# Performance work log

Hardware: AMD Instinct MI355X
Metric: run time of the kernel (lower is better)

## Reference

```python
import jax, jax.numpy as jnp
import numpy as np

DMODEL = 1024
NUM_HEADS = 16
HEAD_DIM = DMODEL // NUM_HEADS


def setup_inputs() -> dict:
    key = jax.random.key(0)
    k_x, k_wqkv, k_bqkv, k_wo, k_bo = jax.random.split(key, 5)
    B, T, D = 4, 2048, DMODEL
    s = 1.0 / np.sqrt(D)
    return {
        "x": jax.random.normal(k_x, (B, T, D), dtype=jnp.float32),
        "w_qkv": jax.random.uniform(k_wqkv, (D, 3 * D), dtype=jnp.float32, minval=-s, maxval=s),
        "b_qkv": jax.random.uniform(k_bqkv, (3 * D,), dtype=jnp.float32, minval=-s, maxval=s),
        "w_out": jax.random.uniform(k_wo, (D, D), dtype=jnp.float32, minval=-s, maxval=s),
        "b_out": jax.random.uniform(k_bo, (D,), dtype=jnp.float32, minval=-s, maxval=s),
    }


def reference(x, w_qkv, b_qkv, w_out, b_out):
    B, T, D = x.shape
    H, Hd = NUM_HEADS, HEAD_DIM
    qkv = x @ w_qkv + b_qkv                      # [B,T,3D]
    qkv = qkv.reshape(B, T, 3, H, Hd)
    q = jnp.transpose(qkv[:, :, 0], (0, 2, 1, 3))  # [B,H,T,Hd]
    k = jnp.transpose(qkv[:, :, 1], (0, 2, 1, 3))
    v = jnp.transpose(qkv[:, :, 2], (0, 2, 1, 3))
    scores = jnp.einsum("bhqd,bhkd->bhqk", q, k) / jnp.sqrt(jnp.float32(Hd))
    weights = jax.nn.softmax(scores, axis=-1)
    attn = jnp.einsum("bhqk,bhkd->bhqd", weights, v)  # [B,H,T,Hd]
    attn = jnp.transpose(attn, (0, 2, 1, 3)).reshape(B, T, D)
    return attn @ w_out + b_out
```

## Files before the change

### kernel.cpp

```cpp
#include <hip/hip_runtime.h>
#include <hip/hip_bf16.h>


typedef __bf16 bf16_t;
typedef __bf16 bf16x8 __attribute__((ext_vector_type(8)));
typedef float f32x4 __attribute__((ext_vector_type(4)));
typedef short short4v __attribute__((ext_vector_type(4)));

#if __has_builtin(__builtin_amdgcn_mfma_f32_16x16x16_bf16)
typedef __bf16 bf16x4 __attribute__((ext_vector_type(4)));
#define MFMA_PV(va, vb, c) __builtin_amdgcn_mfma_f32_16x16x16_bf16( \
    __builtin_bit_cast(bf16x4, (va)), __builtin_bit_cast(bf16x4, (vb)), (c), 0, 0, 0)
#else
#define MFMA_PV(va, vb, c) __builtin_amdgcn_mfma_f32_16x16x16bf16_1k((va), (vb), (c), 0, 0, 0)
#endif

#define DMODEL 1024
#define NH     16
#define HD     64
#define BATCH  4
#define SEQ    2048
#define NTOK   (BATCH * SEQ)
#define NOUT   (NTOK * DMODEL)
#define CEXP   0.1803368801111204f

__device__ __forceinline__ void async_ld16(void* lds, const void* g) {
  __builtin_amdgcn_global_load_lds(
      (const __attribute__((address_space(1))) void*)g,
      (__attribute__((address_space(3))) void*)lds, 16, 0, 0);
}

__global__ __launch_bounds__(256) void sniff_dtype(
    const uint4* __restrict__ x, int* __restrict__ flag,
    const void* __restrict__ sq, const void* __restrict__ so,
    float* __restrict__ dq, float* __restrict__ dofs) {
  int t = threadIdx.x;
  int nanish = 0, zc = 0;
  for (int j = 0; j < 4; ++j) {
    uint4 w = x[t + j * 256];
    unsigned u[4] = {w.x, w.y, w.z, w.w};
    for (int k = 0; k < 4; ++k) {
      unsigned lo = u[k] & 0xFFFFu, hi = u[k] >> 16;
      if ((lo & 0x7F80u) == 0x7F80u) nanish++;
      if ((hi & 0x7F80u) == 0x7F80u) nanish++;
      if (lo == 0) zc++;
      if (hi == 0) zc++;
    }
  }
  __shared__ int rn[256], rz[256];
  rn[t] = nanish; rz[t] = zc;
  __syncthreads();
  for (int s = 128; s > 0; s >>= 1) {
    if (t < s) { rn[t] += rn[t + s]; rz[t] += rz[t + s]; }
    __syncthreads();
  }
  const int f = (rn[0] > 4 || rz[0] > 2048) ? 1 : 0;
  if (t == 0) flag[0] = f;
  for (int j = 0; j < 16; ++j) {
    int i = j * 256 + t;
    if (i < 3072)
      dq[i] = f ? ((const float*)sq)[i] : (float)((const bf16_t*)sq)[i];
    else {
      int k = i - 3072;
      dofs[k] = f ? ((const float*)so)[k] : (float)((const bf16_t*)so)[k];
    }
  }
}

__global__ __launch_bounds__(256) void conv_to_bf16(
    const void* __restrict__ src, bf16_t* __restrict__ dst, int n,
    const int* __restrict__ flag) {
  int i = (blockIdx.x * 256 + threadIdx.x) * 8;
  if (i >= n) return;
  if (flag[0]) {
    const float4* s = (const float4*)((const float*)src + i);
    float4 a = s[0], b = s[1];
    bf16_t* o = dst + i;
    o[0] = (bf16_t)a.x; o[1] = (bf16_t)a.y; o[2] = (bf16_t)a.z; o[3] = (bf16_t)a.w;
    o[4] = (bf16_t)b.x; o[5] = (bf16_t)b.y; o[6] = (bf16_t)b.z; o[7] = (bf16_t)b.w;
  } else {
    *(uint4*)(dst + i) = *(const uint4*)((const bf16_t*)src + i);
  }
}

__global__ __launch_bounds__(256) void transpose_w2(
    const void* __restrict__ in0, bf16_t* __restrict__ out0,
    const void* __restrict__ in1, bf16_t* __restrict__ out1,
    const int* __restrict__ flag) {
  __shared__ bf16_t tile[32][33];
  const int tx = threadIdx.x & 31, ty = threadIdx.x >> 5;
  const bool second = blockIdx.x >= 96;
  const void* in = second ? in1 : in0;
  bf16_t* out = second ? out1 : out0;
  const int C = second ? 1024 : 3072;
  const int R = 1024;
  const int c0 = (second ? (blockIdx.x - 96) : blockIdx.x) * 32;
  const int r0 = blockIdx.y * 32;
  if (flag[0]) {
    for (int i = 0; i < 4; ++i) {
      int r = ty + i * 8;
      tile[r][tx] = (bf16_t)((const float*)in)[(size_t)(r0 + r) * C + c0 + tx];
    }
  } else {
    for (int i = 0; i < 4; ++i) {
      int r = ty + i * 8;
      tile[r][tx] = ((const bf16_t*)in)[(size_t)(r0 + r) * C + c0 + tx];
    }
  }
  __syncthreads();
  for (int i = 0; i < 4; ++i) {
    int r = ty + i * 8;
    out[(size_t)(c0 + r) * R + r0 + tx] = tile[tx][r];
  }
}

template <int MODE>
__global__ __launch_bounds__(256) void gemm_bt_bias(
    const bf16_t* __restrict__ A, const bf16_t* __restrict__ Bt,
    const float* __restrict__ bias, void* __restrict__ Cout,
    int M, int N, int K, const int* __restrict__ flag) {
  __shared__ bf16_t sA[2][128 * 32];
  __shared__ bf16_t sB[2][128 * 32];
  const int t = threadIdx.x;
  const int wave = t >> 6, lane = t & 63;
  const int quad = lane >> 4, l16 = lane & 15;
  const int nwg = gridDim.x * gridDim.y;
  const int lin = blockIdx.y * gridDim.x + blockIdx.x;
  const int cpx = nwg >> 3;
  const int swz = (lin & 7) * cpx + (lin >> 3);
  const int bx = swz % gridDim.x, by = swz / gridDim.x;
  const int bM = by * 128, bN = bx * 128;
  const int m0w = (wave >> 1) * 64, n0w = (wave & 1) * 64;
  const int rowS = wave * 16 + (lane >> 2);
  const int kcS = (lane & 3) * 8;

  f32x4 acc[4][4] = {};

  auto stage = [&](int buf, int k0) {
    for (int r = 0; r < 2; ++r) {
      int row = r * 64 + rowS;
      async_ld16((char*)sA[buf] + r * 4096 + wave * 1024,
                 A + (size_t)(bM + row) * K + k0 + kcS);
      async_ld16((char*)sB[buf] + r * 4096 + wave * 1024,
                 Bt + (size_t)(bN + row) * K + k0 + kcS);
    }
  };

  const int nsteps = K >> 5;
  stage(0, 0);

  for (int s = 0; s < nsteps; ++s) {
    const int cur = s & 1;
    if (s + 1 < nsteps) {
      stage(cur ^ 1, (s + 1) << 5);
      asm volatile("s_waitcnt vmcnt(4)" ::: "memory");
    } else {
      asm volatile("s_waitcnt vmcnt(0)" ::: "memory");
    }
    __builtin_amdgcn_s_barrier();
    asm volatile("" ::: "memory");

    bf16x8 af[4], bfr[4];
    for (int i = 0; i < 4; ++i)
      af[i] = *(const bf16x8*)&sA[cur][(m0w + i * 16 + l16) * 32 + quad * 8];
    for (int j = 0; j < 4; ++j)
      bfr[j] = *(const bf16x8*)&sB[cur][(n0w + j * 16 + l16) * 32 + quad * 8];
    for (int i = 0; i < 4; ++i)
      for (int j = 0; j < 4; ++j)
        acc[i][j] = __builtin_amdgcn_mfma_f32_16x16x32_bf16(af[i], bfr[j], acc[i][j], 0, 0, 0);

    asm volatile("" ::: "memory");
    __builtin_amdgcn_s_barrier();
  }

  const bool f32out = (MODE == 1) && flag[0];
  for (int j = 0; j < 4; ++j) {
    int col = bN + n0w + j * 16 + l16;
    float bv = bias[col];
    for (int i = 0; i < 4; ++i) {
      int row0 = bM + m0w + i * 16 + quad * 4;
      for (int r = 0; r < 4; ++r) {
        float v = acc[i][j][r] + bv;
        if (f32out) ((float*)Cout)[(size_t)(row0 + r) * N + col] = v;
        else        ((bf16_t*)Cout)[(size_t)(row0 + r) * N + col] = (bf16_t)v;
      }
    }
  }
}

__global__ __launch_bounds__(512) void gemm256_qkv(
    const bf16_t* __restrict__ A, const bf16_t* __restrict__ Bt,
    const float* __restrict__ bias, bf16_t* __restrict__ Cout,
    int M, int N, int K, bf16_t* __restrict__ vT) {
  __shared__ __align__(16) char smem[131072];
  char* lds = smem;
  const int t = threadIdx.x;
  const int wave = t >> 6, lane = t & 63;
  const int quad = lane >> 4, l16 = lane & 15;
  const int wr = wave >> 2, wc = wave & 3;
  const int nwg = gridDim.x * gridDim.y;
  const int lin = blockIdx.y * gridDim.x + blockIdx.x;
  const int cpx = nwg >> 3;
  const int swzb = (lin & 7) * cpx + (lin >> 3);
  const int bx = swzb % gridDim.x, by = swzb / gridDim.x;
  const int bM = by * 256, bN = bx * 256;

  const int srow = t >> 2;
  const int xr = ((srow >> 3) & 1) | (((srow >> 2) & 1) << 1);
  const int skl = ((t ^ xr) & 3) * 8;
  const size_t offA0 = (size_t)(bM + srow) * K + skl;
  const size_t offB0 = (size_t)(bN + srow) * K + skl;
  const size_t off1 = (size_t)128 * K;
  const int ldsw = wave * 1024;

#define STG_A(bufo, h, k0t) do {                                               \
    async_ld16(lds + (bufo) + (h) * 16384 + ldsw, A + offA0 + (k0t) + (h) * 32);\
    async_ld16(lds + (bufo) + (h) * 16384 + 8192 + ldsw,                       \
               A + offA0 + off1 + (k0t) + (h) * 32); } while (0)
#define STG_B(bufo, h, k0t) do {                                               \
    async_ld16(lds + (bufo) + 32768 + (h) * 16384 + ldsw,                      \
               Bt + offB0 + (k0t) + (h) * 32);                                 \
    async_ld16(lds + (bufo) + 32768 + (h) * 16384 + 8192 + ldsw,               \
               Bt + offB0 + off1 + (k0t) + (h) * 32); } while (0)

  int aoff[8], boff[4];
#pragma unroll
  for (int mf = 0; mf < 8; ++mf) {
    int r = wr * 128 + mf * 16 + l16;
    aoff[mf] = ((r << 6) + (quad << 4)) ^ (((r & 8) << 1) | ((r & 4) << 3));
  }
#pragma unroll
  for (int nf = 0; nf < 4; ++nf) {
    int r = wc * 64 + nf * 16 + l16;
    boff[nf] = 32768 + (((r << 6) + (quad << 4)) ^ (((r & 8) << 1) | ((r & 4) << 3)));
  }

  f32x4 acc[8][4] = {};
  bf16x8 af[4], bf[4];

#define LDA_SET(mfb, h, bufo) do {                                             \
    af[0] = *(const bf16x8*)(lds + (bufo) + (h) * 16384 + aoff[(mfb) + 0]);    \
    af[1] = *(const bf16x8*)(lds + (bufo) + (h) * 16384 + aoff[(mfb) + 1]);    \
    af[2] = *(const bf16x8*)(lds + (bufo) + (h) * 16384 + aoff[(mfb) + 2]);    \
    af[3] = *(const bf16x8*)(lds + (bufo) + (h) * 16384 + aoff[(mfb) + 3]); } while (0)
#define LDB_SET(h, bufo) do {                                                  \
    bf[0] = *(const bf16x8*)(lds + (bufo) + (h) * 16384 + boff[0]);            \
    bf[1] = *(const bf16x8*)(lds + (bufo) + (h) * 16384 + boff[1]);            \
    bf[2] = *(const bf16x8*)(lds + (bufo) + (h) * 16384 + boff[2]);            \
    bf[3] = *(const bf16x8*)(lds + (bufo) + (h) * 16384 + boff[3]); } while (0)
#define MFMA16(mfb) do {                                                       \
    _Pragma("unroll") for (int i_ = 0; i_ < 4; ++i_)                           \
      { _Pragma("unroll") for (int j_ = 0; j_ < 4; ++j_)                       \
        acc[(mfb) + i_][j_] = __builtin_amdgcn_mfma_f32_16x16x32_bf16(         \
            af[i_], bf[j_], acc[(mfb) + i_][j_], 0, 0, 0); } } while (0)
#define BAR1() do { __builtin_amdgcn_s_barrier(); asm volatile("" ::: "memory"); \
    __builtin_amdgcn_s_setprio(1); } while (0)
#define BAR2() do { __builtin_amdgcn_s_setprio(0);                             \
    asm volatile("" ::: "memory"); __builtin_amdgcn_s_barrier(); } while (0)

  const int NT = K >> 6;
  STG_A(0, 0, 0); STG_B(0, 0, 0); STG_A(0, 1, 0); STG_B(0, 1, 0);
  STG_A(65536, 0, 64); STG_B(65536, 0, 64);
  asm volatile("s_waitcnt vmcnt(4)" ::: "memory");
  __builtin_amdgcn_s_barrier();
  asm volatile("" ::: "memory");

  for (int T = 0; T < NT; ++T) {
    const int bufo = (T & 1) << 16;
    const int obufo = bufo ^ 65536;
    const int k1 = (T + 1) << 6, k2 = (T + 2) << 6;
    LDA_SET(0, 0, bufo); LDB_SET(0, bufo);
    if (T + 1 < NT) STG_A(obufo, 1, k1);
    BAR1(); MFMA16(0); BAR2();
    LDA_SET(4, 0, bufo);
    if (T + 1 < NT) STG_B(obufo, 1, k1);
    BAR1(); MFMA16(4); BAR2();
    LDA_SET(0, 1, bufo); LDB_SET(1, bufo);
    if (T + 2 < NT) STG_A(bufo, 0, k2);
    BAR1(); MFMA16(0); BAR2();
    LDA_SET(4, 1, bufo);
    if (T + 2 < NT) {
      STG_B(bufo, 0, k2);
      asm volatile("s_waitcnt vmcnt(4)" ::: "memory");
    } else {
      asm volatile("s_waitcnt vmcnt(0)" ::: "memory");
    }
    BAR1(); MFMA16(4); BAR2();
  }

#pragma unroll
  for (int nf = 0; nf < 4; ++nf) {
    int col = bN + wc * 64 + nf * 16 + l16;
    float bv = bias[col];
#pragma unroll
    for (int mf = 0; mf < 8; ++mf) {
      int row0 = bM + wr * 128 + mf * 16 + quad * 4;
      if (col >= 2048) {
        int hh = (col - 2048) >> 6, dd = (col - 2048) & 63;
        bf16_t o4[4];
        for (int r = 0; r < 4; ++r) o4[r] = (bf16_t)(acc[mf][nf][r] + bv);
        size_t dst = ((((size_t)(row0 >> 11) * NH + hh) * HD + dd) << 11) | (row0 & 2047);
        *(uint2*)&vT[dst] = *(uint2*)o4;
      } else {
        float scale = (col < 1024) ? CEXP : 1.0f;
        for (int r = 0; r < 4; ++r)
          Cout[(size_t)(row0 + r) * N + col] = (bf16_t)((acc[mf][nf][r] + bv) * scale);
      }
    }
  }
#undef STG_A
#undef STG_B
#undef LDA_SET
#undef LDB_SET
#undef MFMA16
#undef BAR1
#undef BAR2
}

__global__ __launch_bounds__(512) void attention_v12(
    const bf16_t* __restrict__ qkv, const bf16_t* __restrict__ vT,
    bf16_t* __restrict__ attn) {
  const int t = threadIdx.x;
  const int wave = t >> 6, lane = t & 63;
  const int quad = lane >> 4, l16 = lane & 15;
  const int bh = blockIdx.x, b = bh >> 4, h = bh & 15;
  const int qw = blockIdx.y * 256 + wave * 32;

  __shared__ bf16_t Kt[2][128 * 64];
  __shared__ bf16_t Vt[2][64 * 128];

  const bf16_t* qglob = qkv + (size_t)b * SEQ * 3072 + h * 64;
  const bf16_t* kglob = qglob + 1024;
  const bf16_t* vglob = vT + (size_t)bh * HD * SEQ;

  bf16x8 qf[2][2];
  for (int s = 0; s < 2; ++s) {
    const bf16_t* qrow = qglob + (size_t)(qw + s * 16 + l16) * 3072 + quad * 8;
    qf[s][0] = *(const bf16x8*)qrow;
    qf[s][1] = *(const bf16x8*)(qrow + 32);
  }

  f32x4 accO[2][4] = {};
  f32x4 lsum[2] = {};
  const short4v ones4 = {(short)0x3F80, (short)0x3F80, (short)0x3F80, (short)0x3F80};

  const int kRow = lane >> 3, kSlot = lane & 7;
  const int vRow = lane >> 4, vSlot = lane & 15;

  auto stageKV = [&](int buf, int kt) {
    for (int j = 0; j < 2; ++j) {
      int keyl = wave * 16 + j * 8 + kRow;
      int gc = kSlot ^ (keyl & 7);
      async_ld16((char*)Kt[buf] + (wave * 16 + j * 8) * 128,
                 kglob + (size_t)(kt + keyl) * 3072 + gc * 8);
    }
    for (int j = 0; j < 2; ++j) {
      int d = wave * 8 + j * 4 + vRow;
      int gc = vSlot ^ (d & 15);
      async_ld16((char*)Vt[buf] + (wave * 8 + j * 4) * 256,
                 vglob + (size_t)d * SEQ + kt + gc * 8);
    }
  };

  stageKV(0, 0);

  for (int ti = 0; ti < SEQ / 128; ++ti) {
    const int buf = ti & 1;
    __syncthreads();
    if (ti + 1 < SEQ / 128) stageKV(buf ^ 1, (ti + 1) * 128);

    const bf16_t* KtB = Kt[buf];
    const bf16_t* VtB = Vt[buf];

    for (int kb = 0; kb < 8; ++kb) {
      const bf16_t* kr = &KtB[(kb * 16 + l16) * 64];
      bf16x8 kf0 = *(const bf16x8*)(kr + ((quad ^ (l16 & 7)) * 8));
      bf16x8 kf1 = *(const bf16x8*)(kr + (((4 + quad) ^ (l16 & 7)) * 8));

      short4v pB[2];
      for (int s = 0; s < 2; ++s) {
        f32x4 z = {0.f, 0.f, 0.f, 0.f};
        f32x4 st = __builtin_amdgcn_mfma_f32_16x16x32_bf16(kf0, qf[s][0], z, 0, 0, 0);
        st = __builtin_amdgcn_mfma_f32_16x16x32_bf16(kf1, qf[s][1], st, 0, 0, 0);
        union { bf16_t hh[4]; short4v s4; } u;
        for (int r = 0; r < 4; ++r) {
          float p = __builtin_amdgcn_exp2f(st[r]);
          u.hh[r] = (bf16_t)p;
        }
        pB[s] = u.s4;
        lsum[s] = MFMA_PV(ones4, pB[s], lsum[s]);
      }

      const int chunkbase = kb * 2 + (quad >> 1);
      const int coff = (quad & 1) * 4;
      for (int db = 0; db < 4; ++db) {
        short4v vf = *(const short4v*)&VtB[(db * 16 + l16) * 128 +
                                           ((chunkbase ^ l16) * 8) + coff];
        for (int s = 0; s < 2; ++s)
          accO[s][db] = MFMA_PV(vf, pB[s], accO[s][db]);
      }
    }
  }

  for (int s = 0; s < 2; ++s) {
    float inv = 1.f / lsum[s][0];
    size_t tok = (size_t)b * SEQ + qw + s * 16 + l16;
    for (int db = 0; db < 4; ++db) {
      bf16_t o4[4];
      for (int r = 0; r < 4; ++r) o4[r] = (bf16_t)(accO[s][db][r] * inv);
      *(uint2*)&attn[tok * DMODEL + h * HD + db * 16 + quad * 4] = *(uint2*)o4;
    }
  }
}

extern "C" void kernel_launch(void* const* d_in, const int* in_sizes, int n_in,
                              void* d_out, int out_size, void* d_ws, size_t ws_size,
                              hipStream_t stream) {
  const void* x     = d_in[0];
  const void* w_qkv = d_in[1];
  const void* b_qkv = d_in[2];
  const void* w_out = d_in[3];
  const void* b_out = d_in[4];

  char* ws = (char*)d_ws;
  int*    flag  = (int*)ws;
  bf16_t* wqkvT = (bf16_t*)(ws + 4096);
  bf16_t* woutT = (bf16_t*)(ws + 6295552);
  float*  bqkvf = (float*)(ws + 8392704);
  float*  boutf = (float*)(ws + 8404992);
  bf16_t* qkv   = (bf16_t*)(ws + 8409088);
  bf16_t* xb    = (bf16_t*)(ws + 58740736);
  bf16_t* attn  = xb;
  bf16_t* vTbuf = (bf16_t*)(ws + 75517952);

  sniff_dtype<<<1, 256, 0, stream>>>((const uint4*)x, flag, b_qkv, b_out,
                                     bqkvf, boutf);

  conv_to_bf16<<<NOUT / 2048, 256, 0, stream>>>(x, xb, NOUT, flag);

  transpose_w2<<<dim3(128, 32), 256, 0, stream>>>(w_qkv, wqkvT, w_out, woutT, flag);

  gemm256_qkv<<<dim3(12, 32), 512, 0, stream>>>(
      xb, wqkvT, bqkvf, qkv, NTOK, 3072, 1024, vTbuf);

  attention_v12<<<dim3(BATCH * NH, SEQ / 256), 512, 0, stream>>>(qkv, vTbuf, attn);

  gemm_bt_bias<1><<<dim3(8, 64), 256, 0, stream>>>(
      attn, woutT, boutf, d_out, NTOK, 1024, 1024, flag);
}
```

Before: 298.2 us.

## Halve attention KV tile to 64 keys and merge conversion with weight transpose

The attention kernel now stages 64-key K/V tiles instead of 128. Shared memory per block drops from 64KB to 32KB, which could allow more resident blocks per CU, at the cost of twice as many loop iterations and barriers. The x-to-bf16 conversion and the weight transposes are also merged into one launch to save a kernel launch.

Result: faster. 291.1 us (-2.4%).

```diff
diff --git a/kernel.cpp b/kernel.cpp
--- a/kernel.cpp
+++ b/kernel.cpp
@@ -67,35 +67,36 @@
   }
 }
 
-__global__ __launch_bounds__(256) void conv_to_bf16(
-    const void* __restrict__ src, bf16_t* __restrict__ dst, int n,
+__global__ __launch_bounds__(256) void conv_and_transpose(
+    const void* __restrict__ x, bf16_t* __restrict__ xb,
+    const void* __restrict__ w0, bf16_t* __restrict__ out0,
+    const void* __restrict__ w1, bf16_t* __restrict__ out1,
     const int* __restrict__ flag) {
-  int i = (blockIdx.x * 256 + threadIdx.x) * 8;
-  if (i >= n) return;
-  if (flag[0]) {
-    const float4* s = (const float4*)((const float*)src + i);
-    float4 a = s[0], b = s[1];
-    bf16_t* o = dst + i;
-    o[0] = (bf16_t)a.x; o[1] = (bf16_t)a.y; o[2] = (bf16_t)a.z; o[3] = (bf16_t)a.w;
-    o[4] = (bf16_t)b.x; o[5] = (bf16_t)b.y; o[6] = (bf16_t)b.z; o[7] = (bf16_t)b.w;
-  } else {
-    *(uint4*)(dst + i) = *(const uint4*)((const bf16_t*)src + i);
-  }
-}
-
-__global__ __launch_bounds__(256) void transpose_w2(
-    const void* __restrict__ in0, bf16_t* __restrict__ out0,
-    const void* __restrict__ in1, bf16_t* __restrict__ out1,
-    const int* __restrict__ flag) {
+  const int bb = blockIdx.x;
+  if (bb < 4096) {
+    int i = (bb * 256 + threadIdx.x) * 8;
+    if (flag[0]) {
+      const float4* s = (const float4*)((const float*)x + i);
+      float4 a = s[0], b = s[1];
+      bf16_t* o = xb + i;
+      o[0] = (bf16_t)a.x; o[1] = (bf16_t)a.y; o[2] = (bf16_t)a.z; o[3] = (bf16_t)a.w;
+      o[4] = (bf16_t)b.x; o[5] = (bf16_t)b.y; o[6] = (bf16_t)b.z; o[7] = (bf16_t)b.w;
+    } else {
+      *(uint4*)(xb + i) = *(const uint4*)((const bf16_t*)x + i);
+    }
+    return;
+  }
   __shared__ bf16_t tile[32][33];
+  const int idx = bb - 4096;
+  const int bxT = idx & 127, byT = idx >> 7;
   const int tx = threadIdx.x & 31, ty = threadIdx.x >> 5;
-  const bool second = blockIdx.x >= 96;
-  const void* in = second ? in1 : in0;
+  const bool second = bxT >= 96;
+  const void* in = second ? w1 : w0;
   bf16_t* out = second ? out1 : out0;
   const int C = second ? 1024 : 3072;
   const int R = 1024;
-  const int c0 = (second ? (blockIdx.x - 96) : blockIdx.x) * 32;
-  const int r0 = blockIdx.y * 32;
+  const int c0 = (second ? (bxT - 96) : bxT) * 32;
+  const int r0 = byT * 32;
   if (flag[0]) {
     for (int i = 0; i < 4; ++i) {
       int r = ty + i * 8;
@@ -317,7 +318,7 @@
 #undef BAR2
 }
 
-__global__ __launch_bounds__(512) void attention_v12(
+__global__ __launch_bounds__(512) void attention_v13(
     const bf16_t* __restrict__ qkv, const bf16_t* __restrict__ vT,
     bf16_t* __restrict__ attn) {
   const int t = threadIdx.x;
@@ -326,8 +327,8 @@
   const int bh = blockIdx.x, b = bh >> 4, h = bh & 15;
   const int qw = blockIdx.y * 256 + wave * 32;
 
-  __shared__ bf16_t Kt[2][128 * 64];
-  __shared__ bf16_t Vt[2][64 * 128];
+  __shared__ bf16_t Kt[2][64 * 64];
+  __shared__ bf16_t Vt[2][64 * 64];
 
   const bf16_t* qglob = qkv + (size_t)b * SEQ * 3072 + h * 64;
   const bf16_t* kglob = qglob + 1024;
@@ -344,35 +345,30 @@
   f32x4 lsum[2] = {};
   const short4v ones4 = {(short)0x3F80, (short)0x3F80, (short)0x3F80, (short)0x3F80};
 
-  const int kRow = lane >> 3, kSlot = lane & 7;
-  const int vRow = lane >> 4, vSlot = lane & 15;
+  const int sRow = lane >> 3, sSlot = lane & 7;
 
   auto stageKV = [&](int buf, int kt) {
-    for (int j = 0; j < 2; ++j) {
-      int keyl = wave * 16 + j * 8 + kRow;
-      int gc = kSlot ^ (keyl & 7);
-      async_ld16((char*)Kt[buf] + (wave * 16 + j * 8) * 128,
-                 kglob + (size_t)(kt + keyl) * 3072 + gc * 8);
-    }
-    for (int j = 0; j < 2; ++j) {
-      int d = wave * 8 + j * 4 + vRow;
-      int gc = vSlot ^ (d & 15);
-      async_ld16((char*)Vt[buf] + (wave * 8 + j * 4) * 256,
-                 vglob + (size_t)d * SEQ + kt + gc * 8);
-    }
+    int keyl = wave * 8 + sRow;
+    int gck = sSlot ^ (keyl & 7);
+    async_ld16((char*)Kt[buf] + wave * 1024,
+               kglob + (size_t)(kt + keyl) * 3072 + gck * 8);
+    int d = wave * 8 + sRow;
+    int gcv = sSlot ^ (d & 7);
+    async_ld16((char*)Vt[buf] + wave * 1024,
+               vglob + (size_t)d * SEQ + kt + gcv * 8);
   };
 
   stageKV(0, 0);
 
-  for (int ti = 0; ti < SEQ / 128; ++ti) {
+  for (int ti = 0; ti < SEQ / 64; ++ti) {
     const int buf = ti & 1;
     __syncthreads();
-    if (ti + 1 < SEQ / 128) stageKV(buf ^ 1, (ti + 1) * 128);
+    if (ti + 1 < SEQ / 64) stageKV(buf ^ 1, (ti + 1) * 64);
 
     const bf16_t* KtB = Kt[buf];
     const bf16_t* VtB = Vt[buf];
 
-    for (int kb = 0; kb < 8; ++kb) {
+    for (int kb = 0; kb < 4; ++kb) {
       const bf16_t* kr = &KtB[(kb * 16 + l16) * 64];
       bf16x8 kf0 = *(const bf16x8*)(kr + ((quad ^ (l16 & 7)) * 8));
       bf16x8 kf1 = *(const bf16x8*)(kr + (((4 + quad) ^ (l16 & 7)) * 8));
@@ -394,8 +390,8 @@
       const int chunkbase = kb * 2 + (quad >> 1);
       const int coff = (quad & 1) * 4;
       for (int db = 0; db < 4; ++db) {
-        short4v vf = *(const short4v*)&VtB[(db * 16 + l16) * 128 +
-                                           ((chunkbase ^ l16) * 8) + coff];
+        short4v vf = *(const short4v*)&VtB[(db * 16 + l16) * 64 +
+                                           ((chunkbase ^ (l16 & 7)) * 8) + coff];
         for (int s = 0; s < 2; ++s)
           accO[s][db] = MFMA_PV(vf, pB[s], accO[s][db]);
       }
@@ -436,14 +432,13 @@
   sniff_dtype<<<1, 256, 0, stream>>>((const uint4*)x, flag, b_qkv, b_out,
                                      bqkvf, boutf);
 
-  conv_to_bf16<<<NOUT / 2048, 256, 0, stream>>>(x, xb, NOUT, flag);
-
-  transpose_w2<<<dim3(128, 32), 256, 0, stream>>>(w_qkv, wqkvT, w_out, woutT, flag);
+  conv_and_transpose<<<8192, 256, 0, stream>>>(x, xb, w_qkv, wqkvT, w_out, woutT,
+                                               flag);
 
   gemm256_qkv<<<dim3(12, 32), 512, 0, stream>>>(
       xb, wqkvT, bqkvf, qkv, NTOK, 3072, 1024, vTbuf);
 
-  attention_v12<<<dim3(BATCH * NH, SEQ / 256), 512, 0, stream>>>(qkv, vTbuf, attn);
+  attention_v13<<<dim3(BATCH * NH, SEQ / 256), 512, 0, stream>>>(qkv, vTbuf, attn);
 
   gemm_bt_bias<1><<<dim3(8, 64), 256, 0, stream>>>(
       attn, woutT, boutf, d_out, NTOK, 1024, 1024, flag);
```

## Shrink QKV GEMM tile to 128x256 with 3-stage pipeline; fuse conversion kernels

Applied to the files above, without the earlier changes.

The QKV projection GEMM moves from 256x256 tiles to 128x256 tiles, doubling the grid to 768 workgroups. The K loop is restructured into half-tile phases with a three-deep async prefetch and a smaller LDS footprint (96KB). This aims to fill the GPU's compute units better than 384 workgroups did and to allow more overlap, at the cost of lower per-tile reuse of B. Separately, the x-to-bf16 conversion and the weight-transpose kernels are merged into one launch to save a kernel launch.

Measured after the change: 280.0 us. -6.1%, faster.

```diff
diff --git a/kernel.cpp b/kernel.cpp
--- a/kernel.cpp
+++ b/kernel.cpp
@@ -67,35 +67,36 @@
   }
 }
 
-__global__ __launch_bounds__(256) void conv_to_bf16(
-    const void* __restrict__ src, bf16_t* __restrict__ dst, int n,
+__global__ __launch_bounds__(256) void conv_and_transpose(
+    const void* __restrict__ x, bf16_t* __restrict__ xb,
+    const void* __restrict__ w0, bf16_t* __restrict__ out0,
+    const void* __restrict__ w1, bf16_t* __restrict__ out1,
     const int* __restrict__ flag) {
-  int i = (blockIdx.x * 256 + threadIdx.x) * 8;
-  if (i >= n) return;
-  if (flag[0]) {
-    const float4* s = (const float4*)((const float*)src + i);
-    float4 a = s[0], b = s[1];
-    bf16_t* o = dst + i;
-    o[0] = (bf16_t)a.x; o[1] = (bf16_t)a.y; o[2] = (bf16_t)a.z; o[3] = (bf16_t)a.w;
-    o[4] = (bf16_t)b.x; o[5] = (bf16_t)b.y; o[6] = (bf16_t)b.z; o[7] = (bf16_t)b.w;
-  } else {
-    *(uint4*)(dst + i) = *(const uint4*)((const bf16_t*)src + i);
-  }
-}
-
-__global__ __launch_bounds__(256) void transpose_w2(
-    const void* __restrict__ in0, bf16_t* __restrict__ out0,
-    const void* __restrict__ in1, bf16_t* __restrict__ out1,
-    const int* __restrict__ flag) {
+  const int bb = blockIdx.x;
+  if (bb < 4096) {
+    int i = (bb * 256 + threadIdx.x) * 8;
+    if (flag[0]) {
+      const float4* s = (const float4*)((const float*)x + i);
+      float4 a = s[0], b = s[1];
+      bf16_t* o = xb + i;
+      o[0] = (bf16_t)a.x; o[1] = (bf16_t)a.y; o[2] = (bf16_t)a.z; o[3] = (bf16_t)a.w;
+      o[4] = (bf16_t)b.x; o[5] = (bf16_t)b.y; o[6] = (bf16_t)b.z; o[7] = (bf16_t)b.w;
+    } else {
+      *(uint4*)(xb + i) = *(const uint4*)((const bf16_t*)x + i);
+    }
+    return;
+  }
   __shared__ bf16_t tile[32][33];
+  const int idx = bb - 4096;
+  const int bxT = idx & 127, byT = idx >> 7;
   const int tx = threadIdx.x & 31, ty = threadIdx.x >> 5;
-  const bool second = blockIdx.x >= 96;
-  const void* in = second ? in1 : in0;
+  const bool second = bxT >= 96;
+  const void* in = second ? w1 : w0;
   bf16_t* out = second ? out1 : out0;
   const int C = second ? 1024 : 3072;
   const int R = 1024;
-  const int c0 = (second ? (blockIdx.x - 96) : blockIdx.x) * 32;
-  const int r0 = blockIdx.y * 32;
+  const int c0 = (second ? (bxT - 96) : bxT) * 32;
+  const int r0 = byT * 32;
   if (flag[0]) {
     for (int i = 0; i < 4; ++i) {
       int r = ty + i * 8;
@@ -188,11 +189,11 @@
   }
 }
 
-__global__ __launch_bounds__(512) void gemm256_qkv(
+__global__ __launch_bounds__(512) void gemm_qkv_v2(
     const bf16_t* __restrict__ A, const bf16_t* __restrict__ Bt,
     const float* __restrict__ bias, bf16_t* __restrict__ Cout,
     int M, int N, int K, bf16_t* __restrict__ vT) {
-  __shared__ __align__(16) char smem[131072];
+  __shared__ __align__(16) char smem[98304];
   char* lds = smem;
   const int t = threadIdx.x;
   const int wave = t >> 6, lane = t & 63;
@@ -203,89 +204,74 @@
   const int cpx = nwg >> 3;
   const int swzb = (lin & 7) * cpx + (lin >> 3);
   const int bx = swzb % gridDim.x, by = swzb / gridDim.x;
-  const int bM = by * 256, bN = bx * 256;
+  const int bM = by * 128, bN = bx * 256;
 
   const int srow = t >> 2;
   const int xr = ((srow >> 3) & 1) | (((srow >> 2) & 1) << 1);
   const int skl = ((t ^ xr) & 3) * 8;
-  const size_t offA0 = (size_t)(bM + srow) * K + skl;
-  const size_t offB0 = (size_t)(bN + srow) * K + skl;
-  const size_t off1 = (size_t)128 * K;
-  const int ldsw = wave * 1024;
-
-#define STG_A(bufo, h, k0t) do {                                               \
-    async_ld16(lds + (bufo) + (h) * 16384 + ldsw, A + offA0 + (k0t) + (h) * 32);\
-    async_ld16(lds + (bufo) + (h) * 16384 + 8192 + ldsw,                       \
-               A + offA0 + off1 + (k0t) + (h) * 32); } while (0)
-#define STG_B(bufo, h, k0t) do {                                               \
-    async_ld16(lds + (bufo) + 32768 + (h) * 16384 + ldsw,                      \
-               Bt + offB0 + (k0t) + (h) * 32);                                 \
-    async_ld16(lds + (bufo) + 32768 + (h) * 16384 + 8192 + ldsw,               \
-               Bt + offB0 + off1 + (k0t) + (h) * 32); } while (0)
-
-  int aoff[8], boff[4];
+  const size_t offA = (size_t)(bM + srow) * K + skl;
+  const size_t offB = (size_t)(bN + srow) * K + skl;
+  const size_t offB2 = offB + (size_t)128 * K;
+
+#define STG(g) do {                                                            \
+    const int tile_ = (g) >> 1, half_ = (g) & 1;                               \
+    const int kk_ = tile_ * 64 + half_ * 32;                                   \
+    char* base_ = lds + ((tile_ & 1) ? 49152 : 0);                             \
+    async_ld16(base_ + half_ * 8192 + t * 16, A + offA + kk_);                 \
+    async_ld16(base_ + 16384 + half_ * 16384 + t * 16, Bt + offB + kk_);       \
+    async_ld16(base_ + 16384 + half_ * 16384 + 8192 + t * 16,                  \
+               Bt + offB2 + kk_); } while (0)
+
+  int aoff[4], boff[4];
 #pragma unroll
-  for (int mf = 0; mf < 8; ++mf) {
-    int r = wr * 128 + mf * 16 + l16;
+  for (int mf = 0; mf < 4; ++mf) {
+    int r = wr * 64 + mf * 16 + l16;
     aoff[mf] = ((r << 6) + (quad << 4)) ^ (((r & 8) << 1) | ((r & 4) << 3));
   }
 #pragma unroll
   for (int nf = 0; nf < 4; ++nf) {
     int r = wc * 64 + nf * 16 + l16;
-    boff[nf] = 32768 + (((r << 6) + (quad << 4)) ^ (((r & 8) << 1) | ((r & 4) << 3)));
-  }
-
-  f32x4 acc[8][4] = {};
-  bf16x8 af[4], bf[4];
-
-#define LDA_SET(mfb, h, bufo) do {                                             \
-    af[0] = *(const bf16x8*)(lds + (bufo) + (h) * 16384 + aoff[(mfb) + 0]);    \
-    af[1] = *(const bf16x8*)(lds + (bufo) + (h) * 16384 + aoff[(mfb) + 1]);    \
-    af[2] = *(const bf16x8*)(lds + (bufo) + (h) * 16384 + aoff[(mfb) + 2]);    \
-    af[3] = *(const bf16x8*)(lds + (bufo) + (h) * 16384 + aoff[(mfb) + 3]); } while (0)
-#define LDB_SET(h, bufo) do {                                                  \
-    bf[0] = *(const bf16x8*)(lds + (bufo) + (h) * 16384 + boff[0]);            \
-    bf[1] = *(const bf16x8*)(lds + (bufo) + (h) * 16384 + boff[1]);            \
-    bf[2] = *(const bf16x8*)(lds + (bufo) + (h) * 16384 + boff[2]);            \
-    bf[3] = *(const bf16x8*)(lds + (bufo) + (h) * 16384 + boff[3]); } while (0)
-#define MFMA16(mfb) do {                                                       \
+    boff[nf] = ((r << 6) + (quad << 4)) ^ (((r & 8) << 1) | ((r & 4) << 3));
+  }
+
+  f32x4 acc[4][4] = {};
+  const int NT = K >> 6;
+
+  STG(0); STG(1); STG(2);
+  asm volatile("s_waitcnt vmcnt(6)" ::: "memory");
+  __builtin_amdgcn_s_barrier();
+  asm volatile("" ::: "memory");
+
+#define PHASE(T, h) do {                                                       \
+    const int bufo_ = ((T) & 1) * 49152;                                       \
+    bf16x8 af[4], bf[4];                                                       \
+    _Pragma("unroll") for (int i_ = 0; i_ < 4; ++i_)                           \
+      af[i_] = *(const bf16x8*)(lds + bufo_ + (h) * 8192 + aoff[i_]);          \
+    _Pragma("unroll") for (int j_ = 0; j_ < 4; ++j_)                           \
+      bf[j_] = *(const bf16x8*)(lds + bufo_ + 16384 + (h) * 16384 + boff[j_]); \
+    const int n_ = 2 * (T) + (h);                                              \
+    if (n_ + 3 < 2 * NT) {                                                     \
+      STG(n_ + 3);                                                             \
+      asm volatile("s_waitcnt vmcnt(6)" ::: "memory");                         \
+    } else if (n_ == 2 * NT - 3) {                                             \
+      asm volatile("s_waitcnt vmcnt(3)" ::: "memory");                         \
+    } else if (n_ == 2 * NT - 2) {                                             \
+      asm volatile("s_waitcnt vmcnt(0)" ::: "memory");                         \
+    }                                                                          \
+    __builtin_amdgcn_s_barrier();                                              \
+    asm volatile("" ::: "memory");                                             \
+    __builtin_amdgcn_s_setprio(1);                                             \
     _Pragma("unroll") for (int i_ = 0; i_ < 4; ++i_)                           \
       { _Pragma("unroll") for (int j_ = 0; j_ < 4; ++j_)                       \
-        acc[(mfb) + i_][j_] = __builtin_amdgcn_mfma_f32_16x16x32_bf16(         \
-            af[i_], bf[j_], acc[(mfb) + i_][j_], 0, 0, 0); } } while (0)
-#define BAR1() do { __builtin_amdgcn_s_barrier(); asm volatile("" ::: "memory"); \
-    __builtin_amdgcn_s_setprio(1); } while (0)
-#define BAR2() do { __builtin_amdgcn_s_setprio(0);                             \
-    asm volatile("" ::: "memory"); __builtin_amdgcn_s_barrier(); } while (0)
-
-  const int NT = K >> 6;
-  STG_A(0, 0, 0); STG_B(0, 0, 0); STG_A(0, 1, 0); STG_B(0, 1, 0);
-  STG_A(65536, 0, 64); STG_B(65536, 0, 64);
-  asm volatile("s_waitcnt vmcnt(4)" ::: "memory");
-  __builtin_amdgcn_s_barrier();
-  asm volatile("" ::: "memory");
+        acc[i_][j_] = __builtin_amdgcn_mfma_f32_16x16x32_bf16(                 \
+            af[i_], bf[j_], acc[i_][j_], 0, 0, 0); }                           \
+    __builtin_amdgcn_s_setprio(0);                                             \
+    asm volatile("" ::: "memory");                                             \
+    __builtin_amdgcn_s_barrier(); } while (0)
 
   for (int T = 0; T < NT; ++T) {
-    const int bufo = (T & 1) << 16;
-    const int obufo = bufo ^ 65536;
-    const int k1 = (T + 1) << 6, k2 = (T + 2) << 6;
-    LDA_SET(0, 0, bufo); LDB_SET(0, bufo);
-    if (T + 1 < NT) STG_A(obufo, 1, k1);
-    BAR1(); MFMA16(0); BAR2();
-    LDA_SET(4, 0, bufo);
-    if (T + 1 < NT) STG_B(obufo, 1, k1);
-    BAR1(); MFMA16(4); BAR2();
-    LDA_SET(0, 1, bufo); LDB_SET(1, bufo);
-    if (T + 2 < NT) STG_A(bufo, 0, k2);
-    BAR1(); MFMA16(0); BAR2();
-    LDA_SET(4, 1, bufo);
-    if (T + 2 < NT) {
-      STG_B(bufo, 0, k2);
-      asm volatile("s_waitcnt vmcnt(4)" ::: "memory");
-    } else {
-      asm volatile("s_waitcnt vmcnt(0)" ::: "memory");
-    }
-    BAR1(); MFMA16(4); BAR2();
+    PHASE(T, 0);
+    PHASE(T, 1);
   }
 
 #pragma unroll
@@ -293,8 +279,8 @@
     int col = bN + wc * 64 + nf * 16 + l16;
     float bv = bias[col];
 #pragma unroll
-    for (int mf = 0; mf < 8; ++mf) {
-      int row0 = bM + wr * 128 + mf * 16 + quad * 4;
+    for (int mf = 0; mf < 4; ++mf) {
+      int row0 = bM + wr * 64 + mf * 16 + quad * 4;
       if (col >= 2048) {
         int hh = (col - 2048) >> 6, dd = (col - 2048) & 63;
         bf16_t o4[4];
@@ -308,13 +294,8 @@
       }
     }
   }
-#undef STG_A
-#undef STG_B
-#undef LDA_SET
-#undef LDB_SET
-#undef MFMA16
-#undef BAR1
-#undef BAR2
+#undef STG
+#undef PHASE
 }
 
 __global__ __launch_bounds__(512) void attention_v12(
@@ -436,11 +417,10 @@
   sniff_dtype<<<1, 256, 0, stream>>>((const uint4*)x, flag, b_qkv, b_out,
                                      bqkvf, boutf);
 
-  conv_to_bf16<<<NOUT / 2048, 256, 0, stream>>>(x, xb, NOUT, flag);
-
-  transpose_w2<<<dim3(128, 32), 256, 0, stream>>>(w_qkv, wqkvT, w_out, woutT, flag);
-
-  gemm256_qkv<<<dim3(12, 32), 512, 0, stream>>>(
+  conv_and_transpose<<<8192, 256, 0, stream>>>(x, xb, w_qkv, wqkvT, w_out, woutT,
+                                               flag);
+
+  gemm_qkv_v2<<<dim3(12, 64), 512, 0, stream>>>(
       xb, wqkvT, bqkvf, qkv, NTOK, 3072, 1024, vTbuf);
 
   attention_v12<<<dim3(BATCH * NH, SEQ / 256), 512, 0, stream>>>(qkv, vTbuf, attn);
```
